# Optimization experiments

Hardware: AMD Instinct MI355X
Metric: run time of the kernel (lower is better)

Reference implementation:

```python
import jax, jax.numpy as jnp
import numpy as np


def exp_segsum(x):
    """exp(segsum(x)) with the -inf mask folded into a zero mask (same math).
    x: (..., T) -> (..., T, T) lower-triangular decay matrix."""
    T = x.shape[-1]
    xr = jnp.broadcast_to(x[..., None], (*x.shape, T))  # (..., d, e) = x[..., d]
    lower = jnp.tril(jnp.ones((T, T), dtype=bool), -1)
    seg = jnp.cumsum(jnp.where(lower, xr, 0.0), axis=-2)
    incl = jnp.tril(jnp.ones((T, T), dtype=bool), 0)
    return jnp.where(incl, jnp.exp(seg), 0.0)


def ssd(x, A, B, C, chunk_size):
    """Mamba2 chunked structured state-space duality.
    x: (b, L, h, p); A: (b, L, h); B, C: (b, L, n) (shared across heads).
    Returns y: (b, L, h, p) and final state (b, h, p, n)."""
    b_, L_, H, P = x.shape
    c = L_ // chunk_size
    xm = x.reshape(b_, c, chunk_size, H, P)                      # b c l h p
    Am = A.reshape(b_, c, chunk_size, H).transpose(0, 3, 1, 2)   # b h c l
    Bm = B.reshape(b_, c, chunk_size, -1)                        # b c l n
    Cm = C.reshape(b_, c, chunk_size, -1)                        # b c l n
    A_cumsum = jnp.cumsum(Am, axis=-1)                           # b h c l
    Lmat = exp_segsum(Am)                                        # b h c l l
    # intra-chunk (diagonal block) outputs
    Y_diag = jnp.einsum('bcln,bcsn,bhcls,bcshp->bclhp', Cm, Bm, Lmat, xm)
    # per-chunk states
    decay_states = jnp.exp(A_cumsum[:, :, :, -1:] - A_cumsum)    # b h c l
    states = jnp.einsum('bcln,bhcl,bclhp->bchpn', Bm, decay_states, xm)
    init = jnp.zeros_like(states[:, :1])
    states = jnp.concatenate([init, states], axis=1)             # b (c+1) h p n
    # inter-chunk recurrence via segsum over chunk-level decays
    decay_chunk = exp_segsum(jnp.pad(A_cumsum[:, :, :, -1], ((0, 0), (0, 0), (1, 0))))
    new_states = jnp.einsum('bhzc,bchpn->bzhpn', decay_chunk, states)
    states, final_state = new_states[:, :-1], new_states[:, -1]
    # state -> output conversion
    decay_out = jnp.exp(A_cumsum)                                # b h c l
    Y_off = jnp.einsum('bcln,bchpn,bhcl->bclhp', Cm, states, decay_out)
    Y = (Y_diag + Y_off).reshape(b_, L_, H, P)
    return Y, final_state


def setup_inputs() -> dict:
    key = jax.random.key(0)
    ks = jax.random.split(key, 4)
    B, L, d_model = 2, 4096, 1024
    expand, head_dim, d_state, d_conv, chunk = 2, 64, 128, 4, 64
    d_inner = d_model * expand           # 2048
    n_heads = d_inner // head_dim        # 32
    d_in_proj = 2 * d_inner + 2 * d_state + n_heads  # 4384
    conv_dim = d_inner + 2 * d_state     # 2304
    x = jax.random.normal(ks[0], (B, L, d_model), jnp.float32)
    in_proj_w = jax.random.normal(ks[1], (d_model, d_in_proj), jnp.float32) / np.sqrt(d_model)
    conv_w = jax.random.normal(ks[2], (d_conv, 1, conv_dim), jnp.float32) * np.sqrt(2.0 / d_conv)
    conv_b = jnp.zeros((conv_dim,), jnp.float32)
    dt_bias = jnp.full((n_heads,), 0.1, jnp.float32)
    A_log = jnp.full((n_heads,), -1.0, jnp.float32)
    D = jnp.full((n_heads,), 0.1, jnp.float32)
    norm_scale = jnp.ones((d_inner,), jnp.float32)
    out_proj_w = jax.random.normal(ks[3], (d_inner, d_model), jnp.float32) / np.sqrt(d_inner)
    return {"x": x, "in_proj_w": in_proj_w, "conv_w": conv_w, "conv_b": conv_b,
            "dt_bias": dt_bias, "A_log": A_log, "D": D, "norm_scale": norm_scale,
            "out_proj_w": out_proj_w, "chunk_size": chunk}


def reference(x, in_proj_w, conv_w, conv_b, dt_bias, A_log, D, norm_scale, out_proj_w, chunk_size):
    n_heads = dt_bias.shape[0]
    d_inner = norm_scale.shape[0]
    head_dim = d_inner // n_heads
    conv_dim = conv_b.shape[0]
    d_state = (conv_dim - d_inner) // 2
    k = conv_w.shape[0]
    A = -jnp.exp(A_log)                                           # (H,)
    zxbcdt = x @ in_proj_w                                        # (B, L, d_in_proj)
    z = zxbcdt[..., :d_inner]
    xbc = zxbcdt[..., d_inner:d_inner + conv_dim]
    dt = jax.nn.softplus(zxbcdt[..., -n_heads:] + dt_bias)       # (B, L, H)
    # causal depthwise conv (pad k-1 both sides then take first L == pad (k-1, 0))
    xbc = jax.lax.conv_general_dilated(
        xbc, conv_w, window_strides=(1,), padding=[(k - 1, 0)],
        dimension_numbers=('NWC', 'WIO', 'NWC'), feature_group_count=conv_dim) + conv_b
    xbc = jax.nn.silu(xbc)
    xs = xbc[..., :d_inner]
    b = xbc[..., d_inner:d_inner + d_state]
    c = xbc[..., d_inner + d_state:]
    xs = xs.reshape(*xs.shape[:2], n_heads, head_dim)            # (B, L, H, P)
    y, ssm_state = ssd(xs * dt[..., None], A * dt, b, c, chunk_size)
    y = y + xs * D[..., None]
    y = y.reshape(*y.shape[:2], d_inner)
    # gated RMSNorm (Mamba2 norm(y, z))
    yz = y * jax.nn.silu(z)
    y = yz * jax.lax.rsqrt(jnp.mean(yz * yz, axis=-1, keepdims=True) + 1e-6) * norm_scale
    return y @ out_proj_w
```

## Files before the change

kernel.cpp:

```cpp
#include <hip/hip_runtime.h>
#include <hip/hip_bf16.h>
#include <math.h>

typedef __hip_bfloat16 bf16;
typedef __attribute__((ext_vector_type(8))) short short8;
typedef __attribute__((ext_vector_type(4))) float f32x4;

constexpr int BB    = 2;
constexpr int LL    = 4096;
constexpr int DM    = 1024;
constexpr int DIN   = 2048;
constexpr int HH    = 32;
constexpr int PP    = 64;
constexpr int NSD   = 128;
constexpr int CONVD = 2304;
constexpr int DPROJ = 4384;
constexpr int NPAD  = 4480;
constexpr int CHK   = 64;
constexpr int NC    = 64;
constexpr int ROWS  = BB * LL;

__device__ __forceinline__ float b2f(bf16 v) { return __bfloat162float(v); }
__device__ __forceinline__ bf16  f2b(float f) { return __float2bfloat16(f); }
__device__ __forceinline__ short f2bs(float f) {
  bf16 b = f2b(f);
  return *reinterpret_cast<short*>(&b);
}
__device__ __forceinline__ void gload16(const short* g, short* l) {
  __builtin_amdgcn_global_load_lds(
      (const __attribute__((address_space(1))) void*)g,
      (__attribute__((address_space(3))) void*)l, 16, 0, 0);
}

__global__ __launch_bounds__(256) void convert_bf16(const float* __restrict__ in,
                                                    bf16* __restrict__ outp, int n4) {
  int i = blockIdx.x * 256 + threadIdx.x;
  if (i >= n4) return;
  float4 v = *(const float4*)&in[(size_t)i * 4];
  bf16* p = &outp[(size_t)i * 4];
  p[0] = f2b(v.x); p[1] = f2b(v.y); p[2] = f2b(v.z); p[3] = f2b(v.w);
}

__global__ __launch_bounds__(256) void transpose_w(const float* __restrict__ W,
                                                   bf16* __restrict__ Bt,
                                                   int K, int N) {
  __shared__ float Tl[32][33];
  const int n0 = blockIdx.x * 32, k0 = blockIdx.y * 32;
  const int t = threadIdx.x;
  {
    const int kk = t >> 3, nn4 = (t & 7) * 4;
#pragma unroll
    for (int j = 0; j < 4; ++j) {
      int n = n0 + nn4 + j;
      Tl[kk][nn4 + j] = (n < N) ? W[(size_t)(k0 + kk) * N + n] : 0.f;
    }
  }
  __syncthreads();
  {
    const int nn = t >> 3, kk4 = (t & 7) * 4;
#pragma unroll
    for (int j = 0; j < 4; ++j)
      Bt[(size_t)(n0 + nn) * K + k0 + kk4 + j] = f2b(Tl[kk4 + j][nn]);
  }
}

template <int MODE>
__global__ __launch_bounds__(256) void gemm_mfma(
    const short* __restrict__ A, const short* __restrict__ Bt, int K,
    bf16* __restrict__ zb, bf16* __restrict__ xbcb,
    float* __restrict__ dtraw, float* __restrict__ Cout) {
  __shared__ short Asl[128 * 32];
  __shared__ short Bsl[128 * 32];
  const int t = threadIdx.x;
  const int l = t & 63;
  const int w = t >> 6;
  const int wr = w >> 1, wc = w & 1;
  const int m0 = blockIdx.y * 128;
  const int n0 = blockIdx.x * 128;
  const int srow = l >> 2;
  const int sk   = (l & 3) * 8;
  f32x4 acc[4][4] = {};

  for (int k0 = 0; k0 < K; k0 += 32) {
#pragma unroll
    for (int i = 0; i < 2; ++i) {
      int rbase = (i * 4 + w) * 16;
      gload16(&A[(size_t)(m0 + rbase + srow) * K + k0 + sk],
              &Asl[rbase * 32]);
      gload16(&Bt[(size_t)(n0 + rbase + srow) * K + k0 + sk],
              &Bsl[rbase * 32]);
    }
    __syncthreads();
    short8 af[4], bg[4];
#pragma unroll
    for (int i = 0; i < 4; ++i) {
      int ar = wr * 64 + i * 16 + (l & 15);
      af[i] = *(const short8*)&Asl[ar * 32 + (l >> 4) * 8];
      int br = wc * 64 + i * 16 + (l & 15);
      bg[i] = *(const short8*)&Bsl[br * 32 + (l >> 4) * 8];
    }
#pragma unroll
    for (int i = 0; i < 4; ++i)
#pragma unroll
      for (int j = 0; j < 4; ++j)
        acc[i][j] = __builtin_amdgcn_mfma_f32_16x16x32_bf16(af[i], bg[j],
                                                            acc[i][j], 0, 0, 0);
    __syncthreads();
  }
#pragma unroll
  for (int i = 0; i < 4; ++i) {
#pragma unroll
    for (int j = 0; j < 4; ++j) {
      int gcol = n0 + wc * 64 + j * 16 + (l & 15);
      int grow0 = m0 + wr * 64 + i * 16 + (l >> 4) * 4;
#pragma unroll
      for (int q = 0; q < 4; ++q) {
        float v = acc[i][j][q];
        int grow = grow0 + q;
        if constexpr (MODE == 0) {
          if (gcol < DIN) {
            zb[(size_t)grow * DIN + gcol] = f2b(v);
          } else if (gcol < DIN + CONVD) {
            xbcb[(size_t)grow * CONVD + (gcol - DIN)] = f2b(v);
          } else if (gcol < DPROJ) {
            dtraw[(size_t)grow * HH + (gcol - DIN - CONVD)] = v;
          }
        } else {
          Cout[(size_t)grow * DM + gcol] = v;
        }
      }
    }
  }
}

__global__ __launch_bounds__(256) void conv_act(
    const bf16* __restrict__ xbc, const float* __restrict__ dtraw,
    const float* __restrict__ convw, const float* __restrict__ convb,
    const float* __restrict__ dtb, const float* __restrict__ alog,
    bf16* __restrict__ xs, bf16* __restrict__ Bb, bf16* __restrict__ Cb,
    float* __restrict__ dtv, float* __restrict__ dtA) {
  const int row = blockIdx.x;
  const int l   = row & (LL - 1);
  const int t   = threadIdx.x;
  if (t < HH) {
    float raw = dtraw[(size_t)row * HH + t] + dtb[t];
    float dt  = (raw > 20.f) ? raw : log1pf(expf(raw));
    dtv[(size_t)row * HH + t] = dt;
    dtA[(size_t)row * HH + t] = -expf(alog[t]) * dt;
  }
  for (int ch = t * 8; ch < CONVD; ch += 2048) {
    float acc[8];
#pragma unroll
    for (int j = 0; j < 8; ++j) acc[j] = convb[ch + j];
#pragma unroll
    for (int k = 0; k < 4; ++k) {
      if (l - 3 + k >= 0) {
        uint4 v = *(const uint4*)&xbc[(size_t)(row - 3 + k) * CONVD + ch];
        const bf16* pv = (const bf16*)&v;
        const float* wp = &convw[k * CONVD + ch];
#pragma unroll
        for (int j = 0; j < 8; ++j) acc[j] += b2f(pv[j]) * wp[j];
      }
    }
    short8 sv;
#pragma unroll
    for (int j = 0; j < 8; ++j) {
      float s = acc[j] / (1.f + expf(-acc[j]));
      sv[j] = f2bs(s);
    }
    if (ch < DIN) {
      *(short8*)&xs[(size_t)row * DIN + ch] = sv;
    } else if (ch < DIN + NSD) {
      *(short8*)&Bb[(size_t)row * NSD + (ch - DIN)] = sv;
    } else {
      *(short8*)&Cb[(size_t)row * NSD + (ch - DIN - NSD)] = sv;
    }
  }
}

__global__ __launch_bounds__(256) void gmat(const bf16* __restrict__ Bb,
                                            const bf16* __restrict__ Cb,
                                            float* __restrict__ G) {
  const int c = blockIdx.x, b = blockIdx.y;
  const int row0 = (b * NC + c) * CHK;
  __shared__ short Csh[64][136];
  __shared__ short Bsh[64][136];
  const int t = threadIdx.x;
  const int lane = t & 63, w = t >> 6;
#pragma unroll
  for (int i = 0; i < 4; ++i) {
    int f = t + i * 256;
    int rr = f >> 4, n0 = (f & 15) * 8;
    *(uint4*)&Csh[rr][n0] = *(const uint4*)&Cb[(size_t)(row0 + rr) * NSD + n0];
    *(uint4*)&Bsh[rr][n0] = *(const uint4*)&Bb[(size_t)(row0 + rr) * NSD + n0];
  }
  __syncthreads();
  f32x4 acc[4] = {};
  const int r = lane & 15, hi = lane >> 4;
#pragma unroll
  for (int kk = 0; kk < 4; ++kk) {
    short8 af = *(const short8*)&Csh[16 * w + r][kk * 32 + hi * 8];
#pragma unroll
    for (int j = 0; j < 4; ++j) {
      short8 bg = *(const short8*)&Bsh[16 * j + r][kk * 32 + hi * 8];
      acc[j] = __builtin_amdgcn_mfma_f32_16x16x32_bf16(af, bg, acc[j], 0, 0, 0);
    }
  }
#pragma unroll
  for (int j = 0; j < 4; ++j)
#pragma unroll
    for (int q = 0; q < 4; ++q) {
      int ll = 16 * w + hi * 4 + q, ss = 16 * j + r;
      G[((size_t)(b * NC + c) * CHK + ll) * CHK + ss] = acc[j][q];
    }
}

__global__ __launch_bounds__(256) void ssd_chunk(
    const float* __restrict__ G, const bf16* __restrict__ xsp,
    const bf16* __restrict__ Bb, const float* __restrict__ dtv,
    const float* __restrict__ dtA,
    bf16* __restrict__ y, bf16* __restrict__ states, float* __restrict__ cumA) {
  const int h = blockIdx.x, c = blockIdx.y, b = blockIdx.z;
  const int row0 = (b * NC + c) * CHK;
  __shared__ short GMb[64][72];
  __shared__ short xdsT[64][72];
  __shared__ short BdT[128][72];
  __shared__ float sA[CHK], cA[CHK], dec[CHK], sdt[CHK];
  const int t = threadIdx.x;
  const int lane = t & 63, w = t >> 6;
  if (t < CHK) {
    sA[t]  = dtA[(size_t)(row0 + t) * HH + h];
    sdt[t] = dtv[(size_t)(row0 + t) * HH + h];
  }
  __syncthreads();
  if (t == 0) {
    float s = 0.f;
    for (int i = 0; i < CHK; ++i) { s += sA[i]; cA[i] = s; }
  }
  __syncthreads();
  if (t < CHK) {
    dec[t] = expf(cA[CHK - 1] - cA[t]);
    cumA[((size_t)(b * HH + h) * NC + c) * CHK + t] = cA[t];
  }
#pragma unroll
  for (int i = 0; i < 2; ++i) {
    int f = t + i * 256;
    int ll = f >> 3, p0 = (f & 7) * 8;
    uint4 v = *(const uint4*)&xsp[(size_t)(row0 + ll) * DIN + h * PP + p0];
    const bf16* pv = (const bf16*)&v;
    float dtl = sdt[ll];
#pragma unroll
    for (int j = 0; j < 8; ++j) xdsT[p0 + j][ll] = f2bs(b2f(pv[j]) * dtl);
  }
#pragma unroll
  for (int i = 0; i < 4; ++i) {
    int f = t + i * 256;
    int ll = f >> 4, s0 = (f & 15) * 4;
    float4 g = *(const float4*)&G[((size_t)(b * NC + c) * CHK + ll) * CHK + s0];
    float ca = cA[ll];
    GMb[ll][s0 + 0] = f2bs((s0 + 0 <= ll) ? g.x * expf(ca - cA[s0 + 0]) : 0.f);
    GMb[ll][s0 + 1] = f2bs((s0 + 1 <= ll) ? g.y * expf(ca - cA[s0 + 1]) : 0.f);
    GMb[ll][s0 + 2] = f2bs((s0 + 2 <= ll) ? g.z * expf(ca - cA[s0 + 2]) : 0.f);
    GMb[ll][s0 + 3] = f2bs((s0 + 3 <= ll) ? g.w * expf(ca - cA[s0 + 3]) : 0.f);
  }
  __syncthreads();
#pragma unroll
  for (int i = 0; i < 4; ++i) {
    int f = t + i * 256;
    int ll = f >> 4, n0 = (f & 15) * 8;
    uint4 v = *(const uint4*)&Bb[(size_t)(row0 + ll) * NSD + n0];
    const bf16* pv = (const bf16*)&v;
    float dl = dec[ll];
#pragma unroll
    for (int j = 0; j < 8; ++j) BdT[n0 + j][ll] = f2bs(b2f(pv[j]) * dl);
  }
  __syncthreads();
  const int r = lane & 15, hi = lane >> 4;
  {
    f32x4 acc[4] = {};
#pragma unroll
    for (int kk = 0; kk < 2; ++kk) {
      short8 af = *(const short8*)&GMb[16 * w + r][kk * 32 + hi * 8];
#pragma unroll
      for (int j = 0; j < 4; ++j) {
        short8 bg = *(const short8*)&xdsT[16 * j + r][kk * 32 + hi * 8];
        acc[j] = __builtin_amdgcn_mfma_f32_16x16x32_bf16(af, bg, acc[j], 0, 0, 0);
      }
    }
#pragma unroll
    for (int j = 0; j < 4; ++j)
#pragma unroll
      for (int q = 0; q < 4; ++q) {
        int ll = 16 * w + hi * 4 + q, pp = 16 * j + r;
        y[(size_t)(row0 + ll) * DIN + h * PP + pp] = f2b(acc[j][q]);
      }
  }
  {
    f32x4 acc[8] = {};
#pragma unroll
    for (int kk = 0; kk < 2; ++kk) {
      short8 af = *(const short8*)&xdsT[16 * w + r][kk * 32 + hi * 8];
#pragma unroll
      for (int j = 0; j < 8; ++j) {
        short8 bg = *(const short8*)&BdT[16 * j + r][kk * 32 + hi * 8];
        acc[j] = __builtin_amdgcn_mfma_f32_16x16x32_bf16(af, bg, acc[j], 0, 0, 0);
      }
    }
    size_t sb = ((size_t)(b * NC + c) * HH + h) * (PP * NSD);
#pragma unroll
    for (int j = 0; j < 8; ++j)
#pragma unroll
      for (int q = 0; q < 4; ++q) {
        int pp = 16 * w + hi * 4 + q, nn = 16 * j + r;
        states[sb + (size_t)pp * NSD + nn] = f2b(acc[j][q]);
      }
  }
}

__global__ __launch_bounds__(256) void scan(bf16* __restrict__ states,
                                            const float* __restrict__ cumA) {
  const int q = blockIdx.x, h = blockIdx.y, b = blockIdx.z;
  const int t = threadIdx.x;
  float S[8] = {};
  for (int c = 0; c < NC; ++c) {
    float tot = expf(cumA[((size_t)(b * HH + h) * NC + c) * CHK + CHK - 1]);
    size_t base = ((size_t)(b * NC + c) * HH + h) * (PP * NSD) + q * 2048 + t;
#pragma unroll
    for (int i = 0; i < 8; ++i) {
      float cs = b2f(states[base + i * 256]);
      states[base + i * 256] = f2b(S[i]);
      S[i] = S[i] * tot + cs;
    }
  }
}

__global__ __launch_bounds__(256) void yoff(
    const bf16* __restrict__ Cb, const bf16* __restrict__ states,
    const float* __restrict__ cumA, const bf16* __restrict__ xs,
    const float* __restrict__ Dp, bf16* __restrict__ y) {
  const int h = blockIdx.x, c = blockIdx.y, b = blockIdx.z;
  const int row0 = (b * NC + c) * CHK;
  __shared__ short Csh[64][136];
  __shared__ short Ssh[64][136];
  __shared__ float dcy[CHK];
  const int t = threadIdx.x;
  const int lane = t & 63, w = t >> 6;
  if (t < CHK) dcy[t] = expf(cumA[((size_t)(b * HH + h) * NC + c) * CHK + t]);
  const size_t sbase = ((size_t)(b * NC + c) * HH + h) * (PP * NSD);
#pragma unroll
  for (int i = 0; i < 4; ++i) {
    int f = t + i * 256;
    int rr = f >> 4, n0 = (f & 15) * 8;
    *(uint4*)&Csh[rr][n0] = *(const uint4*)&Cb[(size_t)(row0 + rr) * NSD + n0];
    *(uint4*)&Ssh[rr][n0] = *(const uint4*)&states[sbase + (size_t)rr * NSD + n0];
  }
  __syncthreads();
  f32x4 acc[4] = {};
  const int r = lane & 15, hi = lane >> 4;
#pragma unroll
  for (int kk = 0; kk < 4; ++kk) {
    short8 af = *(const short8*)&Csh[16 * w + r][kk * 32 + hi * 8];
#pragma unroll
    for (int j = 0; j < 4; ++j) {
      short8 bg = *(const short8*)&Ssh[16 * j + r][kk * 32 + hi * 8];
      acc[j] = __builtin_amdgcn_mfma_f32_16x16x32_bf16(af, bg, acc[j], 0, 0, 0);
    }
  }
  const float Dh = Dp[h];
#pragma unroll
  for (int j = 0; j < 4; ++j)
#pragma unroll
    for (int q = 0; q < 4; ++q) {
      int ll = 16 * w + hi * 4 + q, pp = 16 * j + r;
      size_t idx = (size_t)(row0 + ll) * DIN + h * PP + pp;
      y[idx] = f2b(b2f(y[idx]) + acc[j][q] * dcy[ll] + b2f(xs[idx]) * Dh);
    }
}

__global__ __launch_bounds__(256) void gatenorm(const bf16* __restrict__ y,
                                                const bf16* __restrict__ zb,
                                                const float* __restrict__ nsc,
                                                bf16* __restrict__ outn) {
  const int row = blockIdx.x, t = threadIdx.x;
  float v[8];
  float ss = 0.f;
#pragma unroll
  for (int i = 0; i < 8; ++i) {
    int ch = t + i * 256;
    float z  = b2f(zb[(size_t)row * DIN + ch]);
    float yv = b2f(y[(size_t)row * DIN + ch]);
    float g  = yv * z / (1.f + expf(-z));
    v[i] = g;
    ss += g * g;
  }
#pragma unroll
  for (int off = 32; off > 0; off >>= 1) ss += __shfl_down(ss, off, 64);
  __shared__ float red[4];
  if ((t & 63) == 0) red[t >> 6] = ss;
  __syncthreads();
  float tot = red[0] + red[1] + red[2] + red[3];
  float r = rsqrtf(tot * (1.f / DIN) + 1e-6f);
#pragma unroll
  for (int i = 0; i < 8; ++i) {
    int ch = t + i * 256;
    outn[(size_t)row * DIN + ch] = f2b(v[i] * r * nsc[ch]);
  }
}

extern "C" void kernel_launch(void* const* d_in, const int* in_sizes, int n_in,
                              void* d_out, int out_size, void* d_ws, size_t ws_size,
                              hipStream_t stream) {
  const float* x     = (const float*)d_in[0];
  const float* inw   = (const float*)d_in[1];
  const float* convw = (const float*)d_in[2];
  const float* convb = (const float*)d_in[3];
  const float* dtb   = (const float*)d_in[4];
  const float* alog  = (const float*)d_in[5];
  const float* Dp    = (const float*)d_in[6];
  const float* nsc   = (const float*)d_in[7];
  const float* outw  = (const float*)d_in[8];
  float* out = (float*)d_out;

  char* p = (char*)d_ws;
  bf16*  zb     = (bf16*)p;  p += (size_t)ROWS * DIN * 2;
  bf16*  xbcb   = (bf16*)p;  p += (size_t)ROWS * CONVD * 2;
  bf16*  y      = xbcb;
  float* dtraw  = (float*)p; p += (size_t)ROWS * HH * 4;
  bf16*  xs     = (bf16*)p;  p += (size_t)ROWS * DIN * 2;
  bf16*  states = (bf16*)p;  p += (size_t)BB * NC * HH * PP * NSD * 2;
  bf16*  normb  = states;
  bf16*  Bb     = (bf16*)p;  p += (size_t)ROWS * NSD * 2;
  bf16*  Cb     = (bf16*)p;  p += (size_t)ROWS * NSD * 2;
  float* dtv    = (float*)p; p += (size_t)ROWS * HH * 4;
  float* dtA    = (float*)p; p += (size_t)ROWS * HH * 4;
  float* cumA   = (float*)p; p += (size_t)BB * HH * NC * CHK * 4;
  float* G      = (float*)p; p += (size_t)BB * NC * CHK * CHK * 4;
  bf16*  xb     = (bf16*)p;  p += (size_t)ROWS * DM * 2;
  bf16*  BtIn   = (bf16*)p;  p += (size_t)NPAD * DM * 2;
  bf16*  BtOut  = xb;

  convert_bf16<<<(ROWS * DM / 4 + 255) / 256, 256, 0, stream>>>(x, xb, ROWS * DM / 4);
  transpose_w<<<dim3(NPAD / 32, DM / 32), 256, 0, stream>>>(inw, BtIn, DM, DPROJ);
  gemm_mfma<0><<<dim3(NPAD / 128, ROWS / 128), 256, 0, stream>>>(
      (const short*)xb, (const short*)BtIn, DM, zb, xbcb, dtraw, nullptr);
  transpose_w<<<dim3(DM / 32, DIN / 32), 256, 0, stream>>>(outw, BtOut, DIN, DM);
  conv_act<<<ROWS, 256, 0, stream>>>(xbcb, dtraw, convw, convb, dtb, alog,
                                     xs, Bb, Cb, dtv, dtA);
  gmat<<<dim3(NC, BB), 256, 0, stream>>>(Bb, Cb, G);
  ssd_chunk<<<dim3(HH, NC, BB), 256, 0, stream>>>(G, xs, Bb, dtv, dtA,
                                                  y, states, cumA);
  scan<<<dim3(4, HH, BB), 256, 0, stream>>>(states, cumA);
  yoff<<<dim3(HH, NC, BB), 256, 0, stream>>>(Cb, states, cumA, xs, Dp, y);
  gatenorm<<<ROWS, 256, 0, stream>>>(y, zb, nsc, normb);
  gemm_mfma<1><<<dim3(DM / 128, ROWS / 128), 256, 0, stream>>>(
      (const short*)normb, (const short*)BtOut, DIN, nullptr, nullptr, nullptr, out);

  (void)in_sizes; (void)n_in; (void)out_size; (void)ws_size;
}
```

Measured before the change: 383.9 us.

## Double-buffer LDS tiles in MFMA GEMM and swizzle LDS layout to cut bank conflicts

The bf16 MFMA GEMM now keeps two LDS buffers per operand and prefetches the next K-tile with direct global-to-LDS loads while computing on the current one. This removes one of the two barriers per iteration and hides global load latency. The LDS column offsets are also XOR-style rotated on both the store and the fragment-read side, so the short8 reads hit different banks. LDS use doubles, which can lower occupancy, and the swizzle on both sides has to match exactly or the results will be wrong.

```diff
diff --git a/kernel.cpp b/kernel.cpp
--- a/kernel.cpp
+++ b/kernel.cpp
@@ -69,35 +69,49 @@
     const short* __restrict__ A, const short* __restrict__ Bt, int K,
     bf16* __restrict__ zb, bf16* __restrict__ xbcb,
     float* __restrict__ dtraw, float* __restrict__ Cout) {
-  __shared__ short Asl[128 * 32];
-  __shared__ short Bsl[128 * 32];
+  __shared__ short Asl[2][128 * 32];
+  __shared__ short Bsl[2][128 * 32];
   const int t = threadIdx.x;
   const int l = t & 63;
   const int w = t >> 6;
   const int wr = w >> 1, wc = w & 1;
   const int m0 = blockIdx.y * 128;
   const int n0 = blockIdx.x * 128;
+
   const int srow = l >> 2;
-  const int sk   = (l & 3) * 8;
+  const int sk   = (((l & 3) - ((l >> 3) & 3)) & 3) * 8;
+  const short* gA0 = &A [(size_t)(m0 + (w    ) * 16 + srow) * K + sk];
+  const short* gA1 = &A [(size_t)(m0 + (4 + w) * 16 + srow) * K + sk];
+  const short* gB0 = &Bt[(size_t)(n0 + (w    ) * 16 + srow) * K + sk];
+  const short* gB1 = &Bt[(size_t)(n0 + (4 + w) * 16 + srow) * K + sk];
+  const int ldsA0 = (w * 16) * 32, ldsA1 = ((4 + w) * 16) * 32;
+
+  const int fr = l & 15;
+  const int s2 = (((l >> 4) + ((fr >> 1) & 3)) & 3) * 8;
+  const int aoff = (wr * 64 + fr) * 32 + s2;
+  const int boff = (wc * 64 + fr) * 32 + s2;
+
   f32x4 acc[4][4] = {};
-
-  for (int k0 = 0; k0 < K; k0 += 32) {
-#pragma unroll
-    for (int i = 0; i < 2; ++i) {
-      int rbase = (i * 4 + w) * 16;
-      gload16(&A[(size_t)(m0 + rbase + srow) * K + k0 + sk],
-              &Asl[rbase * 32]);
-      gload16(&Bt[(size_t)(n0 + rbase + srow) * K + k0 + sk],
-              &Bsl[rbase * 32]);
-    }
-    __syncthreads();
+  const int nt = K >> 5;
+
+  gload16(gA0, &Asl[0][ldsA0]); gload16(gA1, &Asl[0][ldsA1]);
+  gload16(gB0, &Bsl[0][ldsA0]); gload16(gB1, &Bsl[0][ldsA1]);
+  gA0 += 32; gA1 += 32; gB0 += 32; gB1 += 32;
+  __syncthreads();
+
+  for (int ti = 0; ti < nt; ++ti) {
+    const int cur = ti & 1;
+    if (ti + 1 < nt) {
+      const int nxt = cur ^ 1;
+      gload16(gA0, &Asl[nxt][ldsA0]); gload16(gA1, &Asl[nxt][ldsA1]);
+      gload16(gB0, &Bsl[nxt][ldsA0]); gload16(gB1, &Bsl[nxt][ldsA1]);
+      gA0 += 32; gA1 += 32; gB0 += 32; gB1 += 32;
+    }
     short8 af[4], bg[4];
 #pragma unroll
     for (int i = 0; i < 4; ++i) {
-      int ar = wr * 64 + i * 16 + (l & 15);
-      af[i] = *(const short8*)&Asl[ar * 32 + (l >> 4) * 8];
-      int br = wc * 64 + i * 16 + (l & 15);
-      bg[i] = *(const short8*)&Bsl[br * 32 + (l >> 4) * 8];
+      af[i] = *(const short8*)&Asl[cur][aoff + i * 512];
+      bg[i] = *(const short8*)&Bsl[cur][boff + i * 512];
     }
 #pragma unroll
     for (int i = 0; i < 4; ++i)
```

Result: faster. 354.7 us (-7.6%).
